# Optimization experiments

Measured on AMD Instinct MI355X. Metric: run time of the kernel, lower is better.

The kernel has to match this reference:

```python
import jax, jax.numpy as jnp
import numpy as np
from jax import lax

T, B, M, N, D, DA, H, W = 32, 8, 256, 256, 684, 512, 12, 48
QC_CH = 512  # hard-coded coverage conv channels in the module


def setup_inputs() -> dict:
    key = jax.random.key(0)
    ks = iter(jax.random.split(key, 64))
    f = lambda shape, s=0.05: jax.random.normal(next(ks), shape, dtype=jnp.float32) * s
    inp = {
        'rembedding': f((T, B, M), 1.0),
        're_embedding': f((T, B, M), 1.0),
        'ly_mask': jnp.ones((T, B), jnp.float32),
        'context': f((B, D, H, W), 1.0),
        'context_mask': jnp.ones((B, H, W), jnp.float32),
        'init_state': f((B, N), 1.0),
        # fc_Wyz/Wyr/Wyh : Linear(2m -> n)
        'Wyz_w': f((N, 2 * M)), 'Wyz_b': jnp.zeros((N,), jnp.float32),
        'Wyr_w': f((N, 2 * M)), 'Wyr_b': jnp.zeros((N,), jnp.float32),
        'Wyh_w': f((N, 2 * M)), 'Wyh_b': jnp.zeros((N,), jnp.float32),
        # fc_Uhz0/Uhr0/Uhh0 : Linear(n -> n, bias=False)
        'Uhz0_w': f((N, N)), 'Uhr0_w': f((N, N)), 'Uhh0_w': f((N, N)),
        # conv_UaC : Conv2d(D, da, 1)
        'UaC_w': f((DA, D)), 'UaC_b': jnp.zeros((DA,), jnp.float32),
        # fc_WaC : Linear(n -> da, bias=False)
        'WaC_w': f((DA, N)),
        # conv_QC : Conv2d(1, 512, 3, padding=1, bias=False)
        'QC_w': f((QC_CH, 1, 3, 3)),
        # fc_UfC : Linear(512 -> da)
        'UfC_w': f((DA, QC_CH)), 'UfC_b': jnp.zeros((DA,), jnp.float32),
        # fc_vaC : Linear(da -> 1)
        'vaC_w': f((1, DA)), 'vaC_b': jnp.zeros((1,), jnp.float32),
        # fc_Uhz2/Uhr2/Uhh2 : Linear(n -> n)
        'Uhz2_w': f((N, N)), 'Uhz2_b': jnp.zeros((N,), jnp.float32),
        'Uhr2_w': f((N, N)), 'Uhr2_b': jnp.zeros((N,), jnp.float32),
        'Uhh2_w': f((N, N)), 'Uhh2_b': jnp.zeros((N,), jnp.float32),
        # fc_Wcz/Wcr/Wch : Linear(D -> n, bias=False)
        'Wcz_w': f((N, D)), 'Wcr_w': f((N, D)), 'Wch_w': f((N, D)),
        # parent positions into the ctC buffer (valid parents are <= current step)
        'rp': jax.random.randint(next(ks), (T, B), 0, T, dtype=jnp.int32),
    }
    return inp


def _forward(rembedding, re_embedding, ly_mask, context, context_mask, init_state,
             Wyz_w, Wyz_b, Wyr_w, Wyr_b, Wyh_w, Wyh_b,
             Uhz0_w, Uhr0_w, Uhh0_w,
             UaC_w, UaC_b, WaC_w, QC_w, UfC_w, UfC_b, vaC_w, vaC_b,
             Uhz2_w, Uhz2_b, Uhr2_w, Uhr2_b, Uhh2_w, Uhh2_b,
             Wcz_w, Wcr_w, Wch_w, rp):
    n_steps, n_samples = rembedding.shape[0], rembedding.shape[1]
    Hc, Wc = context.shape[2], context.shape[3]
    n = init_state.shape[1]
    d = context.shape[1]

    # pctx_ = conv_UaC(context).permute(2,3,0,1)  -> [H, W, B, da]
    pctx = jnp.einsum('bdhw,ad->hwba', context, UaC_w) + UaC_b
    cmask = context_mask.transpose(1, 2, 0)  # [H, W, B]

    emb = jnp.concatenate([rembedding, re_embedding], axis=2)  # [T, B, 2m]
    sbz = emb @ Wyz_w.T + Wyz_b
    sbr = emb @ Wyr_w.T + Wyr_b
    sbh = emb @ Wyh_w.T + Wyh_b

    batch_idx = jnp.arange(n_samples)

    def step(carry, xs):
        h_, ap_, buf = carry  # h_: [B,n], ap_: [B,H,W], buf: [T+1,B,D]
        z_i, r_i, hh_i, lm, rpos, i = xs
        # gather parent contexts from the running ctC buffer (before this step)
        ctP = buf[rpos, batch_idx]  # [B, D]
        # first GRU cell
        z0 = jax.nn.sigmoid(h_ @ Uhz0_w.T + z_i)
        r0 = jax.nn.sigmoid(h_ @ Uhr0_w.T + r_i)
        h0p = jnp.tanh((h_ @ Uhh0_w.T) * r0 + hh_i)
        h0 = z0 * h_ + (1.0 - z0) * h0p
        h0 = lm[:, None] * h0 + (1.0 - lm)[:, None] * h_
        # coverage attention
        query = h0 @ WaC_w.T  # [B, da]
        cover = lax.conv_general_dilated(
            ap_[:, None, :, :], QC_w, (1, 1), ((1, 1), (1, 1)),
            dimension_numbers=('NCHW', 'OIHW', 'NCHW'))  # [B,512,H,W]
        ccov = jnp.einsum('bchw,ac->hwba', cover, UfC_w) + UfC_b  # [H,W,B,da]
        score = jnp.tanh(pctx + query[None, None, :, :] + ccov)  # [H,W,B,da]
        alpha = (score @ vaC_w.T + vaC_b)[..., 0]  # [H,W,B]
        alpha = jnp.exp(alpha - jnp.max(alpha))
        alpha = alpha * cmask
        alpha = alpha / jnp.sum(alpha, axis=(0, 1))[None, None, :] + 1e-10
        alpha_bhw = alpha.transpose(2, 0, 1)  # [B,H,W]
        ap = ap_ + alpha_bhw
        ctC = jnp.einsum('bdhw,bhw->bd', context, alpha_bhw)  # [B, D]
        # second GRU cell conditioned on the context vector
        z2 = jax.nn.sigmoid(h0 @ Uhz2_w.T + Uhz2_b + ctC @ Wcz_w.T)
        r2 = jax.nn.sigmoid(h0 @ Uhr2_w.T + Uhr2_b + ctC @ Wcr_w.T)
        h2p = jnp.tanh((h0 @ Uhh2_w.T + Uhh2_b) * r2 + ctC @ Wch_w.T)
        h2 = z2 * h0 + (1.0 - z2) * h2p
        h2 = lm[:, None] * h2 + (1.0 - lm)[:, None] * h0
        buf = lax.dynamic_update_slice_in_dim(buf, ctC[None], i + 1, axis=0)
        return (h2, ap, buf), (h2, ctC, ctP, alpha_bhw, ap)

    ap0 = jnp.zeros((n_samples, Hc, Wc), rembedding.dtype)
    buf0 = jnp.zeros((n_steps + 1, n_samples, d), rembedding.dtype)
    xs = (sbz, sbr, sbh, ly_mask, rp, jnp.arange(n_steps))
    _, (h2ts, ctCs, ctPs, calphas, calpha_pasts) = lax.scan(
        step, (init_state, ap0, buf0), xs)
    return h2ts, ctCs, ctPs, calphas, calpha_pasts


def reference(rembedding, re_embedding, ly_mask, context, context_mask, init_state,
              Wyz_w, Wyz_b, Wyr_w, Wyr_b, Wyh_w, Wyh_b,
              Uhz0_w, Uhr0_w, Uhh0_w,
              UaC_w, UaC_b, WaC_w, QC_w, UfC_w, UfC_b, vaC_w, vaC_b,
              Uhz2_w, Uhz2_b, Uhr2_w, Uhr2_b, Uhh2_w, Uhh2_b,
              Wcz_w, Wcr_w, Wch_w, rp):
    return _forward(rembedding, re_embedding, ly_mask, context, context_mask, init_state,
                    Wyz_w, Wyz_b, Wyr_w, Wyr_b, Wyh_w, Wyh_b,
                    Uhz0_w, Uhr0_w, Uhh0_w,
                    UaC_w, UaC_b, WaC_w, QC_w, UfC_w, UfC_b, vaC_w, vaC_b,
                    Uhz2_w, Uhz2_b, Uhr2_w, Uhr2_b, Uhh2_w, Uhh2_b,
                    Wcz_w, Wcr_w, Wch_w, rp)
```

## Files before the change

### kernel.cpp

```cpp
#include <hip/hip_runtime.h>
#include <stdint.h>

typedef unsigned short u16;
typedef unsigned int   u32;

#define TB_ 8
#define NN_ 256
#define DD_ 684
#define PP_ 576

#define OFF_SB    0u
#define OFF_TRAN  0u
#define OFF_BUF   786432u
#define OFF_PCTX  1486848u
#define OFF_FKT   10924032u
#define OFF_RAWP  10942464u
#define OFF_H     11237376u
#define OFF_H0    11245568u
#define OFF_EAL   11253760u
#define OFF_SYNC  11272192u
#define OFF_FLG   11276288u
#define WS_NEED   11276304u

#define OFF_H2   0
// ... 198 lines not shown
    const void* __restrict__ Wh, const void* __restrict__ bhh,
    float* __restrict__ sb,
    float* __restrict__ buf, u32* __restrict__ sync, float* __restrict__ h,
    const void* __restrict__ init_state,
    const int* __restrict__ flag)
{
  const int f32 = flag[0];
  const int tid = threadIdx.x;
  int bid = blockIdx.x;
  if (bid < 768){
    __shared__ float emb[512];
    int g = bid >> 8;
    int tb = bid & 255; int t = tb >> 3; int b = tb & 7;
    emb[tid]     = gld(remb,   (size_t)(t*8+b)*256 + tid, f32);
    emb[tid+256] = gld(re_emb, (size_t)(t*8+b)*256 + tid, f32);
    __syncthreads();
    const void* W = (g==0?Wz:(g==1?Wr:Wh));
    const void* bias = (g==0?bz:(g==1?br:bhh));
    float acc = gld(bias, tid, f32) + dotw(W, (size_t)tid*512, emb, 512, f32);
    sb[(((size_t)g*32+t)*8+b)*256 + tid] = acc;
    return;
  }
  bid -= 768;
  {
    int i = bid*256 + tid;
    int stride = 256*256;
    for (int k=i; k<32*TB_*DD_; k+=stride) buf[k] = 0.f;
    for (int k=i; k<TB_*128;    k+=stride) sync[k] = 0u;
    for (int k=i; k<TB_*NN_;    k+=stride) h[k]   = gld(init_state, k, f32);
  }
}


__global__ __launch_bounds__(256, 1) void k_main(
    const void* __restrict__ ly_mask, const void* __restrict__ context, const void* __restrict__ cmask,
    const void* __restrict__ Uhz0, const void* __restrict__ Uhr0, const void* __restrict__ Uhh0,
    const void* __restrict__ WaC, const void* __restrict__ vaC_w, const void* __restrict__ vaC_b,
    const void* __restrict__ Uhz2, const void* __restrict__ Uhz2_b,
    const void* __restrict__ Uhr2, const void* __restrict__ Uhr2_b,
    const void* __restrict__ Uhh2, const void* __restrict__ Uhh2_b,
    const void* __restrict__ Wcz, const void* __restrict__ Wcr, const void* __restrict__ Wch,
    const int* __restrict__ rp,
    const float* __restrict__ pctx, const float* __restrict__ sb, const float* __restrict__ FKt,
    float* buf, float* h_ws, float* h0_ws, float* rawp, u32* syncg,
    float* out, const int* __restrict__ flag)
{
  const int f32 = flag[0];
  const int tid = threadIdx.x;
  const int b = blockIdx.x >> 4;
  const int j = blockIdx.x & 15;
  const int abase = j*32, nbase = j*16;

  __shared__ float hprev[NN_], h0_lds[NN_];
  __shared__ float ap_lds[PP_], al_lds[PP_], cm_lds[PP_];
  __shared__ float ctc_lds[DD_];
  __shared__ float fk_lds[9*32], vac_lds[32], q_lds[32], qpart[256];
  __shared__ float g1[48], u2l[48], wcl[48];
  __shared__ float red[4];

  for (int k=tid; k<288; k+=256) fk_lds[k] = FKt[(k>>5)*512 + abase + (k&31)];
  if (tid < 32) vac_lds[tid] = gld(vaC_w, abase + tid, f32);
  cm_lds[tid]     = gld(cmask, b*PP_ + tid, f32);
  cm_lds[tid+256] = gld(cmask, b*PP_ + tid + 256, f32);
  if (tid < 64) cm_lds[tid+512] = gld(cmask, b*PP_ + tid + 512, f32);
  ap_lds[tid] = 0.f; ap_lds[tid+256] = 0.f;
  if (tid < 64) ap_lds[tid+512] = 0.f;
  const float vb = gld(vaC_b, 0, f32);

  u32* ctr = syncg + b*128;
  u32 bar_t = 0;
  const int p0 = tid, p1 = tid + 256, p2 = tid + 512;
  const bool has3 = (tid < 64);
  const int pown = j*36;

  for (int t=0; t<32; t++){
    const float lm = gld(ly_mask, t*8+b, f32);

    hprev[tid] = aload(&h_ws[b*256 + tid]);
    __syncthreads();
    if (tid < 192){
      int item = tid >> 2, q = tid & 3;
      int g = item >> 4, nl = item & 15;
      int n = nbase + nl;
      const void* U = (g==0 ? Uhz0 : (g==1 ? Uhr0 : Uhh0));
      float acc = dotw(U, (size_t)n*256 + q*64, &hprev[q*64], 64, f32);
      acc += __shfl_xor(acc,1,64); acc += __shfl_xor(acc,2,64);
      if (q==0) g1[g*16+nl] = acc;
    }
    __syncthreads();
    if (tid < 16){
      int n = nbase + tid;
      float hp = hprev[n];
      float z0 = sigm(g1[tid]    + sb[(((size_t)t)*8+b)*256 + n]);
      float r0 = sigm(g1[16+tid] + sb[(((size_t)(32+t))*8+b)*256 + n]);
      float hc = tanh_c(g1[32+tid]*r0 + sb[(((size_t)(64+t))*8+b)*256 + n]);
      float h0v = z0*hp + (1.f - z0)*hc;
      h0v = lm*h0v + (1.f - lm)*hp;
      astore(&h0_ws[b*256 + n], h0v);
    }
    {
      int rpos = rp[t*8+b];
      if ((unsigned)rpos > 31u) rpos = 31;
      int dbase = j*43, dcnt = (j==15) ? 39 : 43;
      if (tid < dcnt){
        int d = dbase + tid;
        out[OFF_CTP + (t*8+b)*DD_ + d] = aload(&buf[((size_t)rpos*8+b)*DD_ + d]);
      }
    }
    bar_t += 16; group_bar(ctr, bar_t);

    h0_lds[tid] = aload(&h0_ws[b*256 + tid]);
    __syncthreads();
    {
      int ai = tid & 31, nb = tid >> 5;
      qpart[nb*32 + ai] = dotw(WaC, (size_t)(abase+ai)*256 + nb*32, &h0_lds[nb*32], 32, f32);
    }
    __syncthreads();
    if (tid < 32){
      float qv = 0.f;
      #pragma unroll
      for (int nb2=0;nb2<8;nb2++) qv += qpart[nb2*32 + tid];
      q_lds[tid] = qv;
    }
    __syncthreads();
    for (int rep=0; rep<3; rep++){
      int p = tid + rep*256;
      if (p >= PP_) break;
      float PQ[32];
      const float* pc = pctx + ((size_t)(b*PP_ + p))*512 + abase;
      #pragma unroll
      for (int q8=0;q8<8;q8++){
        float4 u = *(const float4*)(pc + q8*4);
        PQ[q8*4+0]=u.x; PQ[q8*4+1]=u.y; PQ[q8*4+2]=u.z; PQ[q8*4+3]=u.w;
      }
      int hh_ = p / 48, ww_ = p - hh_*48;
      #pragma unroll
      for (int kh=0;kh<3;kh++){
        int h2_ = hh_ + kh - 1;
        if ((unsigned)h2_ >= 12u) continue;
        #pragma unroll
        for (int kw=0;kw<3;kw++){
          int w2_ = ww_ + kw - 1;
          if ((unsigned)w2_ >= 48u) continue;
          float av = ap_lds[h2_*48 + w2_];
          const float* fkp = &fk_lds[(kh*3+kw)*32];
          #pragma unroll
          for (int ai=0;ai<32;ai++) PQ[ai] = fmaf(av, fkp[ai], PQ[ai]);
        }
      }
      float racc = 0.f;
      #pragma unroll
      for (int ai=0;ai<32;ai++)
        racc = fmaf(vac_lds[ai], tanh_c(PQ[ai] + q_lds[ai]), racc);
      astore(&rawp[((size_t)(b*16+j))*PP_ + p], racc);
    }
    if (tid < 192){
      int item = tid >> 2, q = tid & 3;
      int g = item >> 4, nl = item & 15;
      int n = nbase + nl;
      const void* U = (g==0 ? Uhz2 : (g==1 ? Uhr2 : Uhh2));
      float acc = dotw(U, (size_t)n*256 + q*64, &h0_lds[q*64], 64, f32);
      acc += __shfl_xor(acc,1,64); acc += __shfl_xor(acc,2,64);
      if (q==0) u2l[g*16+nl] = acc;
    }
    bar_t += 16; group_bar(ctr, bar_t);

    {
      float psum = 0.f;
      for (int rep=0; rep<3; rep++){
        int p = tid + rep*256;
        if (p >= PP_) break;
        float raw = vb;
        #pragma unroll
        for (int j2=0;j2<16;j2++) raw += aload(&rawp[((size_t)(b*16+j2))*PP_ + p]);
        raw = fminf(fmaxf(raw, -60.f), 60.f);
        float e = __expf(raw) * cm_lds[p];
        al_lds[p] = e; psum += e;
      }
      #pragma unroll
      for (int off=1; off<64; off<<=1) psum += __shfl_xor(psum, off, 64);
      if ((tid & 63)==0) red[tid>>6] = psum;
    }
    __syncthreads();
    {
      float S = red[0] + red[1] + red[2] + red[3];
      S = fmaxf(S, 1e-30f);
      float inv = rcpf(S);
      float a0 = al_lds[p0]*inv + 1e-10f; al_lds[p0] = a0; ap_lds[p0] += a0;
      float a1 = al_lds[p1]*inv + 1e-10f; al_lds[p1] = a1; ap_lds[p1] += a1;
      if (has3){ float a2 = al_lds[p2]*inv + 1e-10f; al_lds[p2] = a2; ap_lds[p2] += a2; }
    }
    __syncthreads();
    if (tid < 36){
      int p = pown + tid;
      out[OFF_AL  + (t*8+b)*PP_ + p] = al_lds[p];
      out[OFF_APO + (t*8+b)*PP_ + p] = ap_lds[p];
    }
    {
      int dbase = j*43, dcnt = (j==15) ? 39 : 43;
      if (tid < dcnt*4){
        int dd = tid >> 2, q = tid & 3, d = dbase + dd;
        float acc;
        if (f32) acc = dotf((const float*)context + ((size_t)(b*DD_+d))*PP_ + q*144, &al_lds[q*144], 144);
        else {
          const u16* crow = (const u16*)context + ((size_t)(b*DD_+d))*PP_ + q*144;
          acc = 0.f;
          #pragma unroll 6
          for (int k=0;k<144;k+=8) acc += dot8(*(const uint4*)(crow+k), &al_lds[q*144+k]);
        }
        acc += __shfl_xor(acc,1,64); acc += __shfl_xor(acc,2,64);
        if (q==0){
          astore(&out[OFF_CTC + (t*8+b)*DD_ + d], acc);
          if (t < 31) astore(&buf[(((size_t)(t+1))*8+b)*DD_ + d], acc);
        }
      }
    }
    bar_t += 16; group_bar(ctr, bar_t);

    for (int k=tid; k<DD_; k+=256) ctc_lds[k] = aload(&out[OFF_CTC + (t*8+b)*DD_ + k]);
    __syncthreads();
    if (tid < 192){
      int item = tid >> 2, q = tid & 3;
      int g = item >> 4, nl = item & 15;
      int n = nbase + nl;
      const void* W = (g==0 ? Wcz : (g==1 ? Wcr : Wch));
      int base = q*176, cnt = (q==3) ? 156 : 176;
      float acc = dotw(W, (size_t)n*DD_ + base, &ctc_lds[base], cnt, f32);
      acc += __shfl_xor(acc,1,64); acc += __shfl_xor(acc,2,64);
      if (q==0) wcl[g*16+nl] = acc;
    }
    __syncthreads();
    if (tid < 16){
      int n = nbase + tid;
      float h0v = h0_lds[n];
      float z2 = sigm(u2l[tid]    + gld(Uhz2_b, n, f32) + wcl[tid]);
      float r2 = sigm(u2l[16+tid] + gld(Uhr2_b, n, f32) + wcl[16+tid]);
      float hc = tanh_c((u2l[32+tid] + gld(Uhh2_b, n, f32))*r2 + wcl[32+tid]);
      float h2v = z2*h0v + (1.f - z2)*hc;
      h2v = lm*h2v + (1.f - lm)*h0v;
      astore(&h_ws[b*256 + n], h2v);
      out[OFF_H2 + (t*8+b)*256 + n] = h2v;
    }
    bar_t += 16; group_bar(ctr, bar_t);
  }
}


extern "C" void kernel_launch(void* const* d_in, const int* in_sizes, int n_in,
                              void* d_out, int out_size, void* d_ws, size_t ws_size,
                              hipStream_t stream){
  (void)in_sizes; (void)n_in; (void)out_size;
  if (ws_size < WS_NEED) return;

  const void* remb       = d_in[0];
  const void* re_emb     = d_in[1];
  const void* ly_mask    = d_in[2];
  const void* context    = d_in[3];
  const void* cmask      = d_in[4];
  const void* init_state = d_in[5];
  const void* Wyz_w = d_in[6];  const void* Wyz_b = d_in[7];
  const void* Wyr_w = d_in[8];  const void* Wyr_b = d_in[9];
  const void* Wyh_w = d_in[10]; const void* Wyh_b = d_in[11];
  const void* Uhz0  = d_in[12];
  const void* Uhr0  = d_in[13];
  const void* Uhh0  = d_in[14];
  const void* UaC_w = d_in[15]; const void* UaC_b = d_in[16];
  const void* WaC_w = d_in[17];
  const void* QC_w  = d_in[18];
  const void* UfC_w = d_in[19]; const void* UfC_b = d_in[20];
  const void* vaC_w = d_in[21]; const void* vaC_b = d_in[22];
  const void* Uhz2  = d_in[23]; const void* Uhz2_b = d_in[24];
  const void* Uhr2  = d_in[25]; const void* Uhr2_b = d_in[26];
  const void* Uhh2  = d_in[27]; const void* Uhh2_b = d_in[28];
  const void* Wcz   = d_in[29];
  const void* Wcr   = d_in[30];
  const void* Wch   = d_in[31];
  const int*  rp    = (const int*)d_in[32];

  char* ws = (char*)d_ws;
  float* sbp   = (float*)(ws + OFF_SB);
  float* UaCT  = (float*)(ws + OFF_TRAN);
  float* buf   = (float*)(ws + OFF_BUF);
  float* pctx  = (float*)(ws + OFF_PCTX);
  float* FKt   = (float*)(ws + OFF_FKT);
  float* rawp  = (float*)(ws + OFF_RAWP);
  float* h_ws  = (float*)(ws + OFF_H);
  float* h0_ws = (float*)(ws + OFF_H0);
  u32*   syncg = (u32*)  (ws + OFF_SYNC);
  int*   flag  = (int*)  (ws + OFF_FLG);
  float* out   = (float*)d_out;

  k_detect<<<1, 256, 0, stream>>>((const u16*)context, flag);
  k_pre1 <<<120, 256, 0, stream>>>(UaC_w, UaCT, QC_w, UfC_w, FKt, flag);
  k_pctx2<<<144, 256, 0, stream>>>(context, UaCT, UaC_b, UfC_b, pctx, flag);
  k_pre2 <<<1024, 256, 0, stream>>>(remb, re_emb, Wyz_w, Wyz_b, Wyr_w, Wyr_b, Wyh_w, Wyh_b, sbp,
                                    buf, syncg, h_ws, init_state, flag);
  k_main <<<128, 256, 0, stream>>>(ly_mask, context, cmask,
                                   Uhz0, Uhr0, Uhh0, WaC_w, vaC_w, vaC_b,
                                   Uhz2, Uhz2_b, Uhr2, Uhr2_b, Uhh2, Uhh2_b,
                                   Wcz, Wcr, Wch, rp,
                                   pctx, sbp, FKt,
                                   buf, h_ws, h0_ws, rawp, syncg, out, flag);
}
```

Before: 1.190 ms.

## Use 4 blocks of 1024 threads per batch to cut cross-block barrier participants

The persistent recurrent kernel changes from 16 blocks of 256 threads per batch item to 4 blocks of 1024 threads. Each block now covers 128 attention dims, 64 hidden units and 171 context dims. The parent-context copy is folded into the first GEMV phase, and the softmax reduction uses 9 waves. The aim is to reduce the cost of the global group barriers (4 arrivals instead of 16) and to give each block more parallel work per step. In exchange, only 32 CUs are used and each block is much larger, which may raise per-CU latency and limit registers per thread.

```diff
diff --git a/kernel.cpp b/kernel.cpp
--- a/kernel.cpp
+++ b/kernel.cpp
@@ -254,7 +254,7 @@
 }
 
 
-__global__ __launch_bounds__(256, 1) void k_main(
+__global__ __launch_bounds__(1024, 1) void k_main(
     const void* __restrict__ ly_mask, const void* __restrict__ context, const void* __restrict__ cmask,
     const void* __restrict__ Uhz0, const void* __restrict__ Uhr0, const void* __restrict__ Uhh0,
     const void* __restrict__ WaC, const void* __restrict__ vaC_w, const void* __restrict__ vaC_b,
@@ -269,87 +269,83 @@
 {
   const int f32 = flag[0];
   const int tid = threadIdx.x;
-  const int b = blockIdx.x >> 4;
-  const int j = blockIdx.x & 15;
-  const int abase = j*32, nbase = j*16;
+  const int b = blockIdx.x >> 2;
+  const int j = blockIdx.x & 3;
+  const int abase = j*128;
+  const int nbase = j*64;
+  const int dbase = j*171;
 
   __shared__ float hprev[NN_], h0_lds[NN_];
   __shared__ float ap_lds[PP_], al_lds[PP_], cm_lds[PP_];
   __shared__ float ctc_lds[DD_];
-  __shared__ float fk_lds[9*32], vac_lds[32], q_lds[32], qpart[256];
-  __shared__ float g1[48], u2l[48], wcl[48];
-  __shared__ float red[4];
-
-  for (int k=tid; k<288; k+=256) fk_lds[k] = FKt[(k>>5)*512 + abase + (k&31)];
-  if (tid < 32) vac_lds[tid] = gld(vaC_w, abase + tid, f32);
-  cm_lds[tid]     = gld(cmask, b*PP_ + tid, f32);
-  cm_lds[tid+256] = gld(cmask, b*PP_ + tid + 256, f32);
-  if (tid < 64) cm_lds[tid+512] = gld(cmask, b*PP_ + tid + 512, f32);
-  ap_lds[tid] = 0.f; ap_lds[tid+256] = 0.f;
-  if (tid < 64) ap_lds[tid+512] = 0.f;
+  __shared__ float fk_lds[9*128], vac_lds[128], q_lds[128], qpart[1024];
+  __shared__ float g1[192], u2l[192], wcl[192];
+  __shared__ float red16[16];
+
+  for (int k=tid; k<9*128; k+=1024) fk_lds[k] = FKt[(k>>7)*512 + abase + (k&127)];
+  if (tid < 128) vac_lds[tid] = gld(vaC_w, abase + tid, f32);
+  if (tid < PP_){
+    cm_lds[tid] = gld(cmask, b*PP_ + tid, f32);
+    ap_lds[tid] = 0.f;
+  }
   const float vb = gld(vaC_b, 0, f32);
 
   u32* ctr = syncg + b*128;
   u32 bar_t = 0;
-  const int p0 = tid, p1 = tid + 256, p2 = tid + 512;
-  const bool has3 = (tid < 64);
-  const int pown = j*36;
 
   for (int t=0; t<32; t++){
     const float lm = gld(ly_mask, t*8+b, f32);
 
-    hprev[tid] = aload(&h_ws[b*256 + tid]);
-    __syncthreads();
-    if (tid < 192){
-      int item = tid >> 2, q = tid & 3;
-      int g = item >> 4, nl = item & 15;
+    if (tid < 256) hprev[tid] = aload(&h_ws[b*256 + tid]);
+    __syncthreads();
+    if (tid < 768){
+      int g = tid >> 8, rem = tid & 255;
+      int nl = rem >> 2, q = rem & 3;
       int n = nbase + nl;
       const void* U = (g==0 ? Uhz0 : (g==1 ? Uhr0 : Uhh0));
       float acc = dotw(U, (size_t)n*256 + q*64, &hprev[q*64], 64, f32);
       acc += __shfl_xor(acc,1,64); acc += __shfl_xor(acc,2,64);
-      if (q==0) g1[g*16+nl] = acc;
-    }
-    __syncthreads();
-    if (tid < 16){
+      if (q==0) g1[g*64+nl] = acc;
+    } else if (tid < 768+171){
+      int rpos = rp[t*8+b];
+      if ((unsigned)rpos > 31u) rpos = 31;
+      int d = dbase + (tid - 768);
+      out[OFF_CTP + (t*8+b)*DD_ + d] = aload(&buf[((size_t)rpos*8+b)*DD_ + d]);
+    }
+    __syncthreads();
+    if (tid < 64){
       int n = nbase + tid;
       float hp = hprev[n];
-      float z0 = sigm(g1[tid]    + sb[(((size_t)t)*8+b)*256 + n]);
-      float r0 = sigm(g1[16+tid] + sb[(((size_t)(32+t))*8+b)*256 + n]);
-      float hc = tanh_c(g1[32+tid]*r0 + sb[(((size_t)(64+t))*8+b)*256 + n]);
+      float z0 = sigm(g1[tid]     + sb[(((size_t)t)*8+b)*256 + n]);
+      float r0 = sigm(g1[64+tid]  + sb[(((size_t)(32+t))*8+b)*256 + n]);
+      float hc = tanh_c(g1[128+tid]*r0 + sb[(((size_t)(64+t))*8+b)*256 + n]);
       float h0v = z0*hp + (1.f - z0)*hc;
       h0v = lm*h0v + (1.f - lm)*hp;
       astore(&h0_ws[b*256 + n], h0v);
     }
+    bar_t += 4; group_bar(ctr, bar_t);
+
+    if (tid < 256) h0_lds[tid] = aload(&h0_ws[b*256 + tid]);
+    __syncthreads();
     {
-      int rpos = rp[t*8+b];
-      if ((unsigned)rpos > 31u) rpos = 31;
-      int dbase = j*43, dcnt = (j==15) ? 39 : 43;
-      if (tid < dcnt){
-        int d = dbase + tid;
-        out[OFF_CTP + (t*8+b)*DD_ + d] = aload(&buf[((size_t)rpos*8+b)*DD_ + d]);
-      }
-    }
-    bar_t += 16; group_bar(ctr, bar_t);
-
-    h0_lds[tid] = aload(&h0_ws[b*256 + tid]);
-    __syncthreads();
-    {
-      int ai = tid & 31, nb = tid >> 5;
-      qpart[nb*32 + ai] = dotw(WaC, (size_t)(abase+ai)*256 + nb*32, &h0_lds[nb*32], 32, f32);
-    }
-    __syncthreads();
-    if (tid < 32){
+      int nb = tid >> 7, ai = tid & 127;
+      qpart[nb*128 + ai] = dotw(WaC, (size_t)(abase+ai)*256 + nb*32, &h0_lds[nb*32], 32, f32);
+    }
+    __syncthreads();
+    if (tid < 128){
       float qv = 0.f;
       #pragma unroll
-      for (int nb2=0;nb2<8;nb2++) qv += qpart[nb2*32 + tid];
+      for (int nb2=0;nb2<8;nb2++) qv += qpart[nb2*128 + tid];
       q_lds[tid] = qv;
     }
     __syncthreads();
-    for (int rep=0; rep<3; rep++){
-      int p = tid + rep*256;
-      if (p >= PP_) break;
+    for (int round=0; round<3; round++){
+      int item = tid + round*1024;
+      if (item >= 2304) break;
+      int p = item >> 2, vs = item & 3;
+      int alb = vs*32;
       float PQ[32];
-      const float* pc = pctx + ((size_t)(b*PP_ + p))*512 + abase;
+      const float* pc = pctx + ((size_t)(b*PP_ + p))*512 + abase + alb;
       #pragma unroll
       for (int q8=0;q8<8;q8++){
         float4 u = *(const float4*)(pc + q8*4);
@@ -365,105 +361,106 @@
           int w2_ = ww_ + kw - 1;
           if ((unsigned)w2_ >= 48u) continue;
           float av = ap_lds[h2_*48 + w2_];
-          const float* fkp = &fk_lds[(kh*3+kw)*32];
+          const float* fkp = &fk_lds[(kh*3+kw)*128 + alb];
           #pragma unroll
           for (int ai=0;ai<32;ai++) PQ[ai] = fmaf(av, fkp[ai], PQ[ai]);
         }
       }
+      const float* ql = &q_lds[alb];
+      const float* vl = &vac_lds[alb];
       float racc = 0.f;
       #pragma unroll
       for (int ai=0;ai<32;ai++)
-        racc = fmaf(vac_lds[ai], tanh_c(PQ[ai] + q_lds[ai]), racc);
-      astore(&rawp[((size_t)(b*16+j))*PP_ + p], racc);
-    }
-    if (tid < 192){
-      int item = tid >> 2, q = tid & 3;
-      int g = item >> 4, nl = item & 15;
+        racc = fmaf(vl[ai], tanh_c(PQ[ai] + ql[ai]), racc);
+      astore(&rawp[((size_t)(b*16 + j*4 + vs))*PP_ + p], racc);
+    }
+    if (tid < 768){
+      int g = tid >> 8, rem = tid & 255;
+      int nl = rem >> 2, q = rem & 3;
       int n = nbase + nl;
       const void* U = (g==0 ? Uhz2 : (g==1 ? Uhr2 : Uhh2));
       float acc = dotw(U, (size_t)n*256 + q*64, &h0_lds[q*64], 64, f32);
       acc += __shfl_xor(acc,1,64); acc += __shfl_xor(acc,2,64);
-      if (q==0) u2l[g*16+nl] = acc;
-    }
-    bar_t += 16; group_bar(ctr, bar_t);
+      if (q==0) u2l[g*64+nl] = acc;
+    }
+    bar_t += 4; group_bar(ctr, bar_t);
 
     {
-      float psum = 0.f;
-      for (int rep=0; rep<3; rep++){
-        int p = tid + rep*256;
-        if (p >= PP_) break;
+      float ev = 0.f;
+      if (tid < PP_){
         float raw = vb;
         #pragma unroll
-        for (int j2=0;j2<16;j2++) raw += aload(&rawp[((size_t)(b*16+j2))*PP_ + p]);
+        for (int j2=0;j2<16;j2++) raw += aload(&rawp[((size_t)(b*16+j2))*PP_ + tid]);
         raw = fminf(fmaxf(raw, -60.f), 60.f);
-        float e = __expf(raw) * cm_lds[p];
-        al_lds[p] = e; psum += e;
-      }
-      #pragma unroll
-      for (int off=1; off<64; off<<=1) psum += __shfl_xor(psum, off, 64);
-      if ((tid & 63)==0) red[tid>>6] = psum;
-    }
-    __syncthreads();
-    {
-      float S = red[0] + red[1] + red[2] + red[3];
+        ev = __expf(raw) * cm_lds[tid];
+        al_lds[tid] = ev;
+      }
+      if (tid < 576){
+        float s = ev;
+        #pragma unroll
+        for (int off=1; off<64; off<<=1) s += __shfl_xor(s, off, 64);
+        if ((tid & 63)==0) red16[tid>>6] = s;
+      }
+    }
+    __syncthreads();
+    if (tid < PP_){
+      float S = 0.f;
+      #pragma unroll
+      for (int k=0;k<9;k++) S += red16[k];
       S = fmaxf(S, 1e-30f);
       float inv = rcpf(S);
-      float a0 = al_lds[p0]*inv + 1e-10f; al_lds[p0] = a0; ap_lds[p0] += a0;
-      float a1 = al_lds[p1]*inv + 1e-10f; al_lds[p1] = a1; ap_lds[p1] += a1;
-      if (has3){ float a2 = al_lds[p2]*inv + 1e-10f; al_lds[p2] = a2; ap_lds[p2] += a2; }
-    }
-    __syncthreads();
-    if (tid < 36){
-      int p = pown + tid;
+      float av = al_lds[tid]*inv + 1e-10f;
+      al_lds[tid] = av; ap_lds[tid] += av;
+    }
+    __syncthreads();
+    if (tid < 144){
+      int p = j*144 + tid;
       out[OFF_AL  + (t*8+b)*PP_ + p] = al_lds[p];
       out[OFF_APO + (t*8+b)*PP_ + p] = ap_lds[p];
     }
-    {
-      int dbase = j*43, dcnt = (j==15) ? 39 : 43;
-      if (tid < dcnt*4){
-        int dd = tid >> 2, q = tid & 3, d = dbase + dd;
-        float acc;
-        if (f32) acc = dotf((const float*)context + ((size_t)(b*DD_+d))*PP_ + q*144, &al_lds[q*144], 144);
-        else {
-          const u16* crow = (const u16*)context + ((size_t)(b*DD_+d))*PP_ + q*144;
-          acc = 0.f;
-          #pragma unroll 6
-          for (int k=0;k<144;k+=8) acc += dot8(*(const uint4*)(crow+k), &al_lds[q*144+k]);
-        }
-        acc += __shfl_xor(acc,1,64); acc += __shfl_xor(acc,2,64);
-        if (q==0){
-          astore(&out[OFF_CTC + (t*8+b)*DD_ + d], acc);
-          if (t < 31) astore(&buf[(((size_t)(t+1))*8+b)*DD_ + d], acc);
-        }
-      }
-    }
-    bar_t += 16; group_bar(ctr, bar_t);
-
-    for (int k=tid; k<DD_; k+=256) ctc_lds[k] = aload(&out[OFF_CTC + (t*8+b)*DD_ + k]);
-    __syncthreads();
-    if (tid < 192){
-      int item = tid >> 2, q = tid & 3;
-      int g = item >> 4, nl = item & 15;
+    if (tid < 684){
+      int dd = tid >> 2, q = tid & 3, d = dbase + dd;
+      float acc;
+      if (f32) acc = dotf((const float*)context + ((size_t)(b*DD_+d))*PP_ + q*144, &al_lds[q*144], 144);
+      else {
+        const u16* crow = (const u16*)context + ((size_t)(b*DD_+d))*PP_ + q*144;
+        acc = 0.f;
+        #pragma unroll 6
+        for (int k=0;k<144;k+=8) acc += dot8(*(const uint4*)(crow+k), &al_lds[q*144+k]);
+      }
+      acc += __shfl_xor(acc,1,64); acc += __shfl_xor(acc,2,64);
+      if (q==0){
+        astore(&out[OFF_CTC + (t*8+b)*DD_ + d], acc);
+        if (t < 31) astore(&buf[(((size_t)(t+1))*8+b)*DD_ + d], acc);
+      }
+    }
+    bar_t += 4; group_bar(ctr, bar_t);
+
+    if (tid < DD_) ctc_lds[tid] = aload(&out[OFF_CTC + (t*8+b)*DD_ + tid]);
+    __syncthreads();
+    if (tid < 768){
+      int g = tid >> 8, rem = tid & 255;
+      int nl = rem >> 2, q = rem & 3;
       int n = nbase + nl;
       const void* W = (g==0 ? Wcz : (g==1 ? Wcr : Wch));
-      int base = q*176, cnt = (q==3) ? 156 : 176;
+      int base = q*172, cnt = (q==3) ? 168 : 172;
       float acc = dotw(W, (size_t)n*DD_ + base, &ctc_lds[base], cnt, f32);
       acc += __shfl_xor(acc,1,64); acc += __shfl_xor(acc,2,64);
-      if (q==0) wcl[g*16+nl] = acc;
-    }
-    __syncthreads();
-    if (tid < 16){
+      if (q==0) wcl[g*64+nl] = acc;
+    }
+    __syncthreads();
+    if (tid < 64){
       int n = nbase + tid;
       float h0v = h0_lds[n];
-      float z2 = sigm(u2l[tid]    + gld(Uhz2_b, n, f32) + wcl[tid]);
-      float r2 = sigm(u2l[16+tid] + gld(Uhr2_b, n, f32) + wcl[16+tid]);
-      float hc = tanh_c((u2l[32+tid] + gld(Uhh2_b, n, f32))*r2 + wcl[32+tid]);
+      float z2 = sigm(u2l[tid]     + gld(Uhz2_b, n, f32) + wcl[tid]);
+      float r2 = sigm(u2l[64+tid]  + gld(Uhr2_b, n, f32) + wcl[64+tid]);
+      float hc = tanh_c((u2l[128+tid] + gld(Uhh2_b, n, f32))*r2 + wcl[128+tid]);
       float h2v = z2*h0v + (1.f - z2)*hc;
       h2v = lm*h2v + (1.f - lm)*h0v;
       astore(&h_ws[b*256 + n], h2v);
       out[OFF_H2 + (t*8+b)*256 + n] = h2v;
     }
-    bar_t += 16; group_bar(ctr, bar_t);
+    bar_t += 4; group_bar(ctr, bar_t);
   }
 }
 
@@ -517,7 +514,7 @@
   k_pctx2<<<144, 256, 0, stream>>>(context, UaCT, UaC_b, UfC_b, pctx, flag);
   k_pre2 <<<1024, 256, 0, stream>>>(remb, re_emb, Wyz_w, Wyz_b, Wyr_w, Wyr_b, Wyh_w, Wyh_b, sbp,
                                     buf, syncg, h_ws, init_state, flag);
-  k_main <<<128, 256, 0, stream>>>(ly_mask, context, cmask,
+  k_main <<<32, 1024, 0, stream>>>(ly_mask, context, cmask,
                                    Uhz0, Uhr0, Uhh0, WaC_w, vaC_w, vaC_b,
                                    Uhz2, Uhz2_b, Uhr2, Uhr2_b, Uhh2, Uhh2_b,
                                    Wcz, Wcr, Wch, rp,
```

Result: slower. 2.813 ms (+136.3%).

## Shrink per-batch block group from 16 to 4 and drop two grid barriers

Applied to the files above, without the earlier changes.

Each batch element now runs on 4 cooperating blocks instead of 16, so the main kernel launches 32 blocks. Every block redundantly computes the full first GRU stage and the full context vector, which removes two of the four cross-block group barriers per timestep. The aim is to cut inter-block sync latency in this latency-bound recurrent loop. The cost is more serial work per block: full 256-length dot products per thread, 9 attention rounds instead of 3, and full 576-length context reductions, all on far fewer CUs.

```diff
diff --git a/kernel.cpp b/kernel.cpp
--- a/kernel.cpp
+++ b/kernel.cpp
@@ -264,24 +264,26 @@
     const void* __restrict__ Wcz, const void* __restrict__ Wcr, const void* __restrict__ Wch,
     const int* __restrict__ rp,
     const float* __restrict__ pctx, const float* __restrict__ sb, const float* __restrict__ FKt,
-    float* buf, float* h_ws, float* h0_ws, float* rawp, u32* syncg,
+    float* buf, float* h_ws, float* rawp, u32* syncg,
     float* out, const int* __restrict__ flag)
 {
   const int f32 = flag[0];
   const int tid = threadIdx.x;
-  const int b = blockIdx.x >> 4;
-  const int j = blockIdx.x & 15;
-  const int abase = j*32, nbase = j*16;
+  const int b = blockIdx.x >> 2;
+  const int j = blockIdx.x & 3;
+  const int abase = j*128;
+  const int nbase = j*64;
+  const int dbase = j*171;
 
   __shared__ float hprev[NN_], h0_lds[NN_];
   __shared__ float ap_lds[PP_], al_lds[PP_], cm_lds[PP_];
   __shared__ float ctc_lds[DD_];
-  __shared__ float fk_lds[9*32], vac_lds[32], q_lds[32], qpart[256];
-  __shared__ float g1[48], u2l[48], wcl[48];
+  __shared__ float fk_lds[9*128], vac_lds[128], q_lds[128], qpart[256];
+  __shared__ float u2l[192], wcl[192];
   __shared__ float red[4];
 
-  for (int k=tid; k<288; k+=256) fk_lds[k] = FKt[(k>>5)*512 + abase + (k&31)];
-  if (tid < 32) vac_lds[tid] = gld(vaC_w, abase + tid, f32);
+  for (int k=tid; k<9*128; k+=256) fk_lds[k] = FKt[(k>>7)*512 + abase + (k&127)];
+  if (tid < 128) vac_lds[tid] = gld(vaC_w, abase + tid, f32);
   cm_lds[tid]     = gld(cmask, b*PP_ + tid, f32);
   cm_lds[tid+256] = gld(cmask, b*PP_ + tid + 256, f32);
   if (tid < 64) cm_lds[tid+512] = gld(cmask, b*PP_ + tid + 512, f32);
@@ -293,63 +295,45 @@
   u32 bar_t = 0;
   const int p0 = tid, p1 = tid + 256, p2 = tid + 512;
   const bool has3 = (tid < 64);
-  const int pown = j*36;
 
   for (int t=0; t<32; t++){
     const float lm = gld(ly_mask, t*8+b, f32);
 
     hprev[tid] = aload(&h_ws[b*256 + tid]);
     __syncthreads();
-    if (tid < 192){
-      int item = tid >> 2, q = tid & 3;
-      int g = item >> 4, nl = item & 15;
-      int n = nbase + nl;
-      const void* U = (g==0 ? Uhz0 : (g==1 ? Uhr0 : Uhh0));
-      float acc = dotw(U, (size_t)n*256 + q*64, &hprev[q*64], 64, f32);
-      acc += __shfl_xor(acc,1,64); acc += __shfl_xor(acc,2,64);
-      if (q==0) g1[g*16+nl] = acc;
-    }
-    __syncthreads();
-    if (tid < 16){
-      int n = nbase + tid;
-      float hp = hprev[n];
-      float z0 = sigm(g1[tid]    + sb[(((size_t)t)*8+b)*256 + n]);
-      float r0 = sigm(g1[16+tid] + sb[(((size_t)(32+t))*8+b)*256 + n]);
-      float hc = tanh_c(g1[32+tid]*r0 + sb[(((size_t)(64+t))*8+b)*256 + n]);
+    {
+      float az = dotw(Uhz0, (size_t)tid*256, hprev, 256, f32);
+      float ar = dotw(Uhr0, (size_t)tid*256, hprev, 256, f32);
+      float ah = dotw(Uhh0, (size_t)tid*256, hprev, 256, f32);
+      float hp = hprev[tid];
+      float z0 = sigm(az + sb[(((size_t)t)*8+b)*256 + tid]);
+      float r0 = sigm(ar + sb[(((size_t)(32+t))*8+b)*256 + tid]);
+      float hc = tanh_c(ah*r0 + sb[(((size_t)(64+t))*8+b)*256 + tid]);
       float h0v = z0*hp + (1.f - z0)*hc;
-      h0v = lm*h0v + (1.f - lm)*hp;
-      astore(&h0_ws[b*256 + n], h0v);
-    }
-    {
+      h0_lds[tid] = lm*h0v + (1.f - lm)*hp;
+    }
+    if (tid < 171){
       int rpos = rp[t*8+b];
       if ((unsigned)rpos > 31u) rpos = 31;
-      int dbase = j*43, dcnt = (j==15) ? 39 : 43;
-      if (tid < dcnt){
-        int d = dbase + tid;
-        out[OFF_CTP + (t*8+b)*DD_ + d] = aload(&buf[((size_t)rpos*8+b)*DD_ + d]);
-      }
-    }
-    bar_t += 16; group_bar(ctr, bar_t);
-
-    h0_lds[tid] = aload(&h0_ws[b*256 + tid]);
-    __syncthreads();
+      int d = dbase + tid;
+      out[OFF_CTP + (t*8+b)*DD_ + d] = aload(&buf[((size_t)rpos*8+b)*DD_ + d]);
+    }
+    __syncthreads();
+
     {
-      int ai = tid & 31, nb = tid >> 5;
-      qpart[nb*32 + ai] = dotw(WaC, (size_t)(abase+ai)*256 + nb*32, &h0_lds[nb*32], 32, f32);
-    }
-    __syncthreads();
-    if (tid < 32){
-      float qv = 0.f;
-      #pragma unroll
-      for (int nb2=0;nb2<8;nb2++) qv += qpart[nb2*32 + tid];
-      q_lds[tid] = qv;
-    }
-    __syncthreads();
-    for (int rep=0; rep<3; rep++){
-      int p = tid + rep*256;
-      if (p >= PP_) break;
+      int ai = tid & 127, half = tid >> 7;
+      qpart[half*128 + ai] = dotw(WaC, (size_t)(abase+ai)*256 + half*128, &h0_lds[half*128], 128, f32);
+    }
+    __syncthreads();
+    if (tid < 128) q_lds[tid] = qpart[tid] + qpart[128+tid];
+    __syncthreads();
+    #pragma unroll 1
+    for (int round=0; round<9; round++){
+      int item = tid + round*256;
+      int p = item >> 2, vs = item & 3;
+      int alb = vs*32;
       float PQ[32];
-      const float* pc = pctx + ((size_t)(b*PP_ + p))*512 + abase;
+      const float* pc = pctx + ((size_t)(b*PP_ + p))*512 + abase + alb;
       #pragma unroll
       for (int q8=0;q8<8;q8++){
         float4 u = *(const float4*)(pc + q8*4);
@@ -365,27 +349,26 @@
           int w2_ = ww_ + kw - 1;
           if ((unsigned)w2_ >= 48u) continue;
           float av = ap_lds[h2_*48 + w2_];
-          const float* fkp = &fk_lds[(kh*3+kw)*32];
+          const float* fkp = &fk_lds[(kh*3+kw)*128 + alb];
           #pragma unroll
           for (int ai=0;ai<32;ai++) PQ[ai] = fmaf(av, fkp[ai], PQ[ai]);
         }
       }
+      const float* ql = &q_lds[alb];
+      const float* vl = &vac_lds[alb];
       float racc = 0.f;
       #pragma unroll
       for (int ai=0;ai<32;ai++)
-        racc = fmaf(vac_lds[ai], tanh_c(PQ[ai] + q_lds[ai]), racc);
-      astore(&rawp[((size_t)(b*16+j))*PP_ + p], racc);
+        racc = fmaf(vl[ai], tanh_c(PQ[ai] + ql[ai]), racc);
+      astore(&rawp[((size_t)(b*16 + j*4 + vs))*PP_ + p], racc);
     }
     if (tid < 192){
-      int item = tid >> 2, q = tid & 3;
-      int g = item >> 4, nl = item & 15;
+      int g = tid >> 6, nl = tid & 63;
       int n = nbase + nl;
       const void* U = (g==0 ? Uhz2 : (g==1 ? Uhr2 : Uhh2));
-      float acc = dotw(U, (size_t)n*256 + q*64, &h0_lds[q*64], 64, f32);
-      acc += __shfl_xor(acc,1,64); acc += __shfl_xor(acc,2,64);
-      if (q==0) u2l[g*16+nl] = acc;
-    }
-    bar_t += 16; group_bar(ctr, bar_t);
+      u2l[g*64+nl] = dotw(U, (size_t)n*256, h0_lds, 256, f32);
+    }
+    bar_t += 4; group_bar(ctr, bar_t);
 
     {
       float psum = 0.f;
@@ -413,57 +396,46 @@
       if (has3){ float a2 = al_lds[p2]*inv + 1e-10f; al_lds[p2] = a2; ap_lds[p2] += a2; }
     }
     __syncthreads();
-    if (tid < 36){
-      int p = pown + tid;
+    if (tid < 144){
+      int p = j*144 + tid;
       out[OFF_AL  + (t*8+b)*PP_ + p] = al_lds[p];
       out[OFF_APO + (t*8+b)*PP_ + p] = ap_lds[p];
     }
-    {
-      int dbase = j*43, dcnt = (j==15) ? 39 : 43;
-      if (tid < dcnt*4){
-        int dd = tid >> 2, q = tid & 3, d = dbase + dd;
-        float acc;
-        if (f32) acc = dotf((const float*)context + ((size_t)(b*DD_+d))*PP_ + q*144, &al_lds[q*144], 144);
-        else {
-          const u16* crow = (const u16*)context + ((size_t)(b*DD_+d))*PP_ + q*144;
-          acc = 0.f;
-          #pragma unroll 6
-          for (int k=0;k<144;k+=8) acc += dot8(*(const uint4*)(crow+k), &al_lds[q*144+k]);
-        }
-        acc += __shfl_xor(acc,1,64); acc += __shfl_xor(acc,2,64);
-        if (q==0){
-          astore(&out[OFF_CTC + (t*8+b)*DD_ + d], acc);
-          if (t < 31) astore(&buf[(((size_t)(t+1))*8+b)*DD_ + d], acc);
-        }
-      }
-    }
-    bar_t += 16; group_bar(ctr, bar_t);
-
-    for (int k=tid; k<DD_; k+=256) ctc_lds[k] = aload(&out[OFF_CTC + (t*8+b)*DD_ + k]);
+    for (int d = tid; d < DD_; d += 256){
+      float acc;
+      if (f32) acc = dotf((const float*)context + ((size_t)(b*DD_+d))*PP_, al_lds, PP_);
+      else {
+        const u16* crow = (const u16*)context + ((size_t)(b*DD_+d))*PP_;
+        acc = 0.f;
+        #pragma unroll 8
+        for (int k=0;k<PP_;k+=8) acc += dot8(*(const uint4*)(crow+k), &al_lds[k]);
+      }
+      ctc_lds[d] = acc;
+      if ((unsigned)(d - dbase) < 171u){
+        astore(&out[OFF_CTC + (t*8+b)*DD_ + d], acc);
+        if (t < 31) astore(&buf[(((size_t)(t+1))*8+b)*DD_ + d], acc);
+      }
+    }
     __syncthreads();
     if (tid < 192){
-      int item = tid >> 2, q = tid & 3;
-      int g = item >> 4, nl = item & 15;
+      int g = tid >> 6, nl = tid & 63;
       int n = nbase + nl;
       const void* W = (g==0 ? Wcz : (g==1 ? Wcr : Wch));
-      int base = q*176, cnt = (q==3) ? 156 : 176;
-      float acc = dotw(W, (size_t)n*DD_ + base, &ctc_lds[base], cnt, f32);
-      acc += __shfl_xor(acc,1,64); acc += __shfl_xor(acc,2,64);
-      if (q==0) wcl[g*16+nl] = acc;
-    }
-    __syncthreads();
-    if (tid < 16){
+      wcl[g*64+nl] = dotw(W, (size_t)n*DD_, ctc_lds, DD_, f32);
+    }
+    __syncthreads();
+    if (tid < 64){
       int n = nbase + tid;
       float h0v = h0_lds[n];
-      float z2 = sigm(u2l[tid]    + gld(Uhz2_b, n, f32) + wcl[tid]);
-      float r2 = sigm(u2l[16+tid] + gld(Uhr2_b, n, f32) + wcl[16+tid]);
-      float hc = tanh_c((u2l[32+tid] + gld(Uhh2_b, n, f32))*r2 + wcl[32+tid]);
+      float z2 = sigm(u2l[tid]     + gld(Uhz2_b, n, f32) + wcl[tid]);
+      float r2 = sigm(u2l[64+tid]  + gld(Uhr2_b, n, f32) + wcl[64+tid]);
+      float hc = tanh_c((u2l[128+tid] + gld(Uhh2_b, n, f32))*r2 + wcl[128+tid]);
       float h2v = z2*h0v + (1.f - z2)*hc;
       h2v = lm*h2v + (1.f - lm)*h0v;
       astore(&h_ws[b*256 + n], h2v);
       out[OFF_H2 + (t*8+b)*256 + n] = h2v;
     }
-    bar_t += 16; group_bar(ctr, bar_t);
+    bar_t += 4; group_bar(ctr, bar_t);
   }
 }
 
@@ -507,7 +479,6 @@
   float* FKt   = (float*)(ws + OFF_FKT);
   float* rawp  = (float*)(ws + OFF_RAWP);
   float* h_ws  = (float*)(ws + OFF_H);
-  float* h0_ws = (float*)(ws + OFF_H0);
   u32*   syncg = (u32*)  (ws + OFF_SYNC);
   int*   flag  = (int*)  (ws + OFF_FLG);
   float* out   = (float*)d_out;
@@ -517,10 +488,10 @@
   k_pctx2<<<144, 256, 0, stream>>>(context, UaCT, UaC_b, UfC_b, pctx, flag);
   k_pre2 <<<1024, 256, 0, stream>>>(remb, re_emb, Wyz_w, Wyz_b, Wyr_w, Wyr_b, Wyh_w, Wyh_b, sbp,
                                     buf, syncg, h_ws, init_state, flag);
-  k_main <<<128, 256, 0, stream>>>(ly_mask, context, cmask,
-                                   Uhz0, Uhr0, Uhh0, WaC_w, vaC_w, vaC_b,
-                                   Uhz2, Uhz2_b, Uhr2, Uhr2_b, Uhh2, Uhh2_b,
-                                   Wcz, Wcr, Wch, rp,
-                                   pctx, sbp, FKt,
-                                   buf, h_ws, h0_ws, rawp, syncg, out, flag);
-}
+  k_main <<<32, 256, 0, stream>>>(ly_mask, context, cmask,
+                                  Uhz0, Uhr0, Uhh0, WaC_w, vaC_w, vaC_b,
+                                  Uhz2, Uhz2_b, Uhr2, Uhr2_b, Uhh2, Uhh2_b,
+                                  Wcz, Wcr, Wch, rp,
+                                  pctx, sbp, FKt,
+                                  buf, h_ws, rawp, syncg, out, flag);
+}
```

After: 4.511 ms. 279% more time.

## Halve blocks per batch group and distribute softmax normalization via workspace

Applied to the files above, without the earlier changes.

Reduces the persistent recurrent kernel from 16 to 8 cooperating blocks per batch element, so each block handles twice as many hidden units, attention channels and context dims. Cross-block group barriers then involve fewer participants. The softmax exponentials are now computed once per position by the owning block and shared through a global buffer with partial sums, instead of every block recomputing all 576 positions. This adds a fourth group barrier per step and gives each block more serial work.

```diff
diff --git a/kernel.cpp b/kernel.cpp
--- a/kernel.cpp
+++ b/kernel.cpp
@@ -264,24 +264,27 @@
     const void* __restrict__ Wcz, const void* __restrict__ Wcr, const void* __restrict__ Wch,
     const int* __restrict__ rp,
     const float* __restrict__ pctx, const float* __restrict__ sb, const float* __restrict__ FKt,
-    float* buf, float* h_ws, float* h0_ws, float* rawp, u32* syncg,
+    float* buf, float* h_ws, float* h0_ws, float* ealpha, float* rawp, u32* syncg,
     float* out, const int* __restrict__ flag)
 {
   const int f32 = flag[0];
   const int tid = threadIdx.x;
-  const int b = blockIdx.x >> 4;
-  const int j = blockIdx.x & 15;
-  const int abase = j*32, nbase = j*16;
+  const int b = blockIdx.x >> 3;
+  const int j = blockIdx.x & 7;
+  const int abase = j*64, nbase = j*32;
+  const int dbase = j*85 + (j < 4 ? j : 4);
+  const int dcnt  = (j < 4) ? 86 : 85;
+  const int pown  = j*72;
 
   __shared__ float hprev[NN_], h0_lds[NN_];
   __shared__ float ap_lds[PP_], al_lds[PP_], cm_lds[PP_];
   __shared__ float ctc_lds[DD_];
-  __shared__ float fk_lds[9*32], vac_lds[32], q_lds[32], qpart[256];
-  __shared__ float g1[48], u2l[48], wcl[48];
-  __shared__ float red[4];
-
-  for (int k=tid; k<288; k+=256) fk_lds[k] = FKt[(k>>5)*512 + abase + (k&31)];
-  if (tid < 32) vac_lds[tid] = gld(vaC_w, abase + tid, f32);
+  __shared__ float fk_lds[9*64], vac_lds[64], q_lds[64], qpart[256];
+  __shared__ float g1[96], u2l[96], wcl[96];
+  __shared__ float red16[16];
+
+  for (int k=tid; k<9*64; k+=256) fk_lds[k] = FKt[(k>>6)*512 + abase + (k&63)];
+  if (tid < 64) vac_lds[tid] = gld(vaC_w, abase + tid, f32);
   cm_lds[tid]     = gld(cmask, b*PP_ + tid, f32);
   cm_lds[tid+256] = gld(cmask, b*PP_ + tid + 256, f32);
   if (tid < 64) cm_lds[tid+512] = gld(cmask, b*PP_ + tid + 512, f32);
@@ -290,10 +293,10 @@
   const float vb = gld(vaC_b, 0, f32);
 
   u32* ctr = syncg + b*128;
+  float* psum_ws = (float*)(ctr + 96);
   u32 bar_t = 0;
   const int p0 = tid, p1 = tid + 256, p2 = tid + 512;
   const bool has3 = (tid < 64);
-  const int pown = j*36;
 
   for (int t=0; t<32; t++){
     const float lm = gld(ly_mask, t*8+b, f32);
@@ -301,21 +304,21 @@
     hprev[tid] = aload(&h_ws[b*256 + tid]);
     __syncthreads();
     if (tid < 192){
-      int item = tid >> 2, q = tid & 3;
-      int g = item >> 4, nl = item & 15;
+      int item = tid >> 1, q = tid & 1;
+      int g = item >> 5, nl = item & 31;
       int n = nbase + nl;
       const void* U = (g==0 ? Uhz0 : (g==1 ? Uhr0 : Uhh0));
-      float acc = dotw(U, (size_t)n*256 + q*64, &hprev[q*64], 64, f32);
-      acc += __shfl_xor(acc,1,64); acc += __shfl_xor(acc,2,64);
-      if (q==0) g1[g*16+nl] = acc;
-    }
-    __syncthreads();
-    if (tid < 16){
+      float acc = dotw(U, (size_t)n*256 + q*128, &hprev[q*128], 128, f32);
+      acc += __shfl_xor(acc,1,64);
+      if (q==0) g1[g*32+nl] = acc;
+    }
+    __syncthreads();
+    if (tid < 32){
       int n = nbase + tid;
       float hp = hprev[n];
       float z0 = sigm(g1[tid]    + sb[(((size_t)t)*8+b)*256 + n]);
-      float r0 = sigm(g1[16+tid] + sb[(((size_t)(32+t))*8+b)*256 + n]);
-      float hc = tanh_c(g1[32+tid]*r0 + sb[(((size_t)(64+t))*8+b)*256 + n]);
+      float r0 = sigm(g1[32+tid] + sb[(((size_t)(32+t))*8+b)*256 + n]);
+      float hc = tanh_c(g1[64+tid]*r0 + sb[(((size_t)(64+t))*8+b)*256 + n]);
       float h0v = z0*hp + (1.f - z0)*hc;
       h0v = lm*h0v + (1.f - lm)*hp;
       astore(&h0_ws[b*256 + n], h0v);
@@ -323,33 +326,33 @@
     {
       int rpos = rp[t*8+b];
       if ((unsigned)rpos > 31u) rpos = 31;
-      int dbase = j*43, dcnt = (j==15) ? 39 : 43;
       if (tid < dcnt){
         int d = dbase + tid;
         out[OFF_CTP + (t*8+b)*DD_ + d] = aload(&buf[((size_t)rpos*8+b)*DD_ + d]);
       }
     }
-    bar_t += 16; group_bar(ctr, bar_t);
+    bar_t += 8; group_bar(ctr, bar_t);
 
     h0_lds[tid] = aload(&h0_ws[b*256 + tid]);
     __syncthreads();
     {
-      int ai = tid & 31, nb = tid >> 5;
-      qpart[nb*32 + ai] = dotw(WaC, (size_t)(abase+ai)*256 + nb*32, &h0_lds[nb*32], 32, f32);
-    }
-    __syncthreads();
-    if (tid < 32){
-      float qv = 0.f;
-      #pragma unroll
-      for (int nb2=0;nb2<8;nb2++) qv += qpart[nb2*32 + tid];
+      int ai = tid & 63, nb = tid >> 6;
+      qpart[nb*64 + ai] = dotw(WaC, (size_t)(abase+ai)*256 + nb*64, &h0_lds[nb*64], 64, f32);
+    }
+    __syncthreads();
+    if (tid < 64){
+      float qv = qpart[tid] + qpart[64+tid] + qpart[128+tid] + qpart[192+tid];
       q_lds[tid] = qv;
     }
     __syncthreads();
-    for (int rep=0; rep<3; rep++){
-      int p = tid + rep*256;
-      if (p >= PP_) break;
+    #pragma unroll 1
+    for (int round=0; round<5; round++){
+      int item = tid + round*256;
+      if (item >= 1152) break;
+      int p = item >> 1, vs = item & 1;
+      int alb = vs*32;
       float PQ[32];
-      const float* pc = pctx + ((size_t)(b*PP_ + p))*512 + abase;
+      const float* pc = pctx + ((size_t)(b*PP_ + p))*512 + abase + alb;
       #pragma unroll
       for (int q8=0;q8<8;q8++){
         float4 u = *(const float4*)(pc + q8*4);
@@ -365,105 +368,117 @@
           int w2_ = ww_ + kw - 1;
           if ((unsigned)w2_ >= 48u) continue;
           float av = ap_lds[h2_*48 + w2_];
-          const float* fkp = &fk_lds[(kh*3+kw)*32];
+          const float* fkp = &fk_lds[(kh*3+kw)*64 + alb];
           #pragma unroll
           for (int ai=0;ai<32;ai++) PQ[ai] = fmaf(av, fkp[ai], PQ[ai]);
         }
       }
+      const float* ql = &q_lds[alb];
+      const float* vl = &vac_lds[alb];
       float racc = 0.f;
       #pragma unroll
       for (int ai=0;ai<32;ai++)
-        racc = fmaf(vac_lds[ai], tanh_c(PQ[ai] + q_lds[ai]), racc);
-      astore(&rawp[((size_t)(b*16+j))*PP_ + p], racc);
+        racc = fmaf(vl[ai], tanh_c(PQ[ai] + ql[ai]), racc);
+      astore(&rawp[((size_t)(b*16 + j*2 + vs))*PP_ + p], racc);
     }
     if (tid < 192){
-      int item = tid >> 2, q = tid & 3;
-      int g = item >> 4, nl = item & 15;
+      int item = tid >> 1, q = tid & 1;
+      int g = item >> 5, nl = item & 31;
       int n = nbase + nl;
       const void* U = (g==0 ? Uhz2 : (g==1 ? Uhr2 : Uhh2));
-      float acc = dotw(U, (size_t)n*256 + q*64, &h0_lds[q*64], 64, f32);
-      acc += __shfl_xor(acc,1,64); acc += __shfl_xor(acc,2,64);
-      if (q==0) u2l[g*16+nl] = acc;
-    }
-    bar_t += 16; group_bar(ctr, bar_t);
+      float acc = dotw(U, (size_t)n*256 + q*128, &h0_lds[q*128], 128, f32);
+      acc += __shfl_xor(acc,1,64);
+      if (q==0) u2l[g*32+nl] = acc;
+    }
+    bar_t += 8; group_bar(ctr, bar_t);
 
     {
-      float psum = 0.f;
-      for (int rep=0; rep<3; rep++){
-        int p = tid + rep*256;
-        if (p >= PP_) break;
+      float ev = 0.f;
+      if (tid < 72){
+        int p = pown + tid;
         float raw = vb;
         #pragma unroll
         for (int j2=0;j2<16;j2++) raw += aload(&rawp[((size_t)(b*16+j2))*PP_ + p]);
         raw = fminf(fmaxf(raw, -60.f), 60.f);
-        float e = __expf(raw) * cm_lds[p];
-        al_lds[p] = e; psum += e;
-      }
-      #pragma unroll
-      for (int off=1; off<64; off<<=1) psum += __shfl_xor(psum, off, 64);
-      if ((tid & 63)==0) red[tid>>6] = psum;
-    }
-    __syncthreads();
+        ev = __expf(raw) * cm_lds[p];
+        astore(&ealpha[b*PP_ + p], ev);
+      }
+      if (tid < 128){
+        float s = ev;
+        #pragma unroll
+        for (int off=1; off<64; off<<=1) s += __shfl_xor(s, off, 64);
+        if ((tid & 63) == 0) astore(&psum_ws[j*2 + (tid>>6)], s);
+      }
+    }
+    bar_t += 8; group_bar(ctr, bar_t);
+
     {
-      float S = red[0] + red[1] + red[2] + red[3];
+      float e0 = aload(&ealpha[b*PP_ + p0]);
+      float e1 = aload(&ealpha[b*PP_ + p1]);
+      float e2 = has3 ? aload(&ealpha[b*PP_ + p2]) : 0.f;
+      if (tid < 16) red16[tid] = aload(&psum_ws[tid]);
+      __syncthreads();
+      float S = 0.f;
+      #pragma unroll
+      for (int k=0;k<16;k++) S += red16[k];
       S = fmaxf(S, 1e-30f);
       float inv = rcpf(S);
-      float a0 = al_lds[p0]*inv + 1e-10f; al_lds[p0] = a0; ap_lds[p0] += a0;
-      float a1 = al_lds[p1]*inv + 1e-10f; al_lds[p1] = a1; ap_lds[p1] += a1;
-      if (has3){ float a2 = al_lds[p2]*inv + 1e-10f; al_lds[p2] = a2; ap_lds[p2] += a2; }
-    }
-    __syncthreads();
-    if (tid < 36){
+      float a0 = e0*inv + 1e-10f; al_lds[p0] = a0; ap_lds[p0] += a0;
+      float a1 = e1*inv + 1e-10f; al_lds[p1] = a1; ap_lds[p1] += a1;
+      if (has3){ float a2 = e2*inv + 1e-10f; al_lds[p2] = a2; ap_lds[p2] += a2; }
+    }
+    __syncthreads();
+    if (tid < 72){
       int p = pown + tid;
       out[OFF_AL  + (t*8+b)*PP_ + p] = al_lds[p];
       out[OFF_APO + (t*8+b)*PP_ + p] = ap_lds[p];
     }
     {
-      int dbase = j*43, dcnt = (j==15) ? 39 : 43;
-      if (tid < dcnt*4){
-        int dd = tid >> 2, q = tid & 3, d = dbase + dd;
+      int dd = tid >> 1, q = tid & 1;
+      if (dd < dcnt){
+        int d = dbase + dd;
         float acc;
-        if (f32) acc = dotf((const float*)context + ((size_t)(b*DD_+d))*PP_ + q*144, &al_lds[q*144], 144);
+        if (f32) acc = dotf((const float*)context + ((size_t)(b*DD_+d))*PP_ + q*288, &al_lds[q*288], 288);
         else {
-          const u16* crow = (const u16*)context + ((size_t)(b*DD_+d))*PP_ + q*144;
+          const u16* crow = (const u16*)context + ((size_t)(b*DD_+d))*PP_ + q*288;
           acc = 0.f;
           #pragma unroll 6
-          for (int k=0;k<144;k+=8) acc += dot8(*(const uint4*)(crow+k), &al_lds[q*144+k]);
+          for (int k=0;k<288;k+=8) acc += dot8(*(const uint4*)(crow+k), &al_lds[q*288+k]);
         }
-        acc += __shfl_xor(acc,1,64); acc += __shfl_xor(acc,2,64);
+        acc += __shfl_xor(acc,1,64);
         if (q==0){
           astore(&out[OFF_CTC + (t*8+b)*DD_ + d], acc);
           if (t < 31) astore(&buf[(((size_t)(t+1))*8+b)*DD_ + d], acc);
         }
       }
     }
-    bar_t += 16; group_bar(ctr, bar_t);
+    bar_t += 8; group_bar(ctr, bar_t);
 
     for (int k=tid; k<DD_; k+=256) ctc_lds[k] = aload(&out[OFF_CTC + (t*8+b)*DD_ + k]);
     __syncthreads();
     if (tid < 192){
-      int item = tid >> 2, q = tid & 3;
-      int g = item >> 4, nl = item & 15;
+      int item = tid >> 1, q = tid & 1;
+      int g = item >> 5, nl = item & 31;
       int n = nbase + nl;
       const void* W = (g==0 ? Wcz : (g==1 ? Wcr : Wch));
-      int base = q*176, cnt = (q==3) ? 156 : 176;
+      int base = q*344, cnt = q ? 340 : 344;
       float acc = dotw(W, (size_t)n*DD_ + base, &ctc_lds[base], cnt, f32);
-      acc += __shfl_xor(acc,1,64); acc += __shfl_xor(acc,2,64);
-      if (q==0) wcl[g*16+nl] = acc;
-    }
-    __syncthreads();
-    if (tid < 16){
+      acc += __shfl_xor(acc,1,64);
+      if (q==0) wcl[g*32+nl] = acc;
+    }
+    __syncthreads();
+    if (tid < 32){
       int n = nbase + tid;
       float h0v = h0_lds[n];
       float z2 = sigm(u2l[tid]    + gld(Uhz2_b, n, f32) + wcl[tid]);
-      float r2 = sigm(u2l[16+tid] + gld(Uhr2_b, n, f32) + wcl[16+tid]);
-      float hc = tanh_c((u2l[32+tid] + gld(Uhh2_b, n, f32))*r2 + wcl[32+tid]);
+      float r2 = sigm(u2l[32+tid] + gld(Uhr2_b, n, f32) + wcl[32+tid]);
+      float hc = tanh_c((u2l[64+tid] + gld(Uhh2_b, n, f32))*r2 + wcl[64+tid]);
       float h2v = z2*h0v + (1.f - z2)*hc;
       h2v = lm*h2v + (1.f - lm)*h0v;
       astore(&h_ws[b*256 + n], h2v);
       out[OFF_H2 + (t*8+b)*256 + n] = h2v;
     }
-    bar_t += 16; group_bar(ctr, bar_t);
+    bar_t += 8; group_bar(ctr, bar_t);
   }
 }
 
@@ -508,6 +523,7 @@
   float* rawp  = (float*)(ws + OFF_RAWP);
   float* h_ws  = (float*)(ws + OFF_H);
   float* h0_ws = (float*)(ws + OFF_H0);
+  float* eal   = (float*)(ws + OFF_EAL);
   u32*   syncg = (u32*)  (ws + OFF_SYNC);
   int*   flag  = (int*)  (ws + OFF_FLG);
   float* out   = (float*)d_out;
@@ -517,10 +533,10 @@
   k_pctx2<<<144, 256, 0, stream>>>(context, UaCT, UaC_b, UfC_b, pctx, flag);
   k_pre2 <<<1024, 256, 0, stream>>>(remb, re_emb, Wyz_w, Wyz_b, Wyr_w, Wyr_b, Wyh_w, Wyh_b, sbp,
                                     buf, syncg, h_ws, init_state, flag);
-  k_main <<<128, 256, 0, stream>>>(ly_mask, context, cmask,
-                                   Uhz0, Uhr0, Uhh0, WaC_w, vaC_w, vaC_b,
-                                   Uhz2, Uhz2_b, Uhr2, Uhr2_b, Uhh2, Uhh2_b,
-                                   Wcz, Wcr, Wch, rp,
-                                   pctx, sbp, FKt,
-                                   buf, h_ws, h0_ws, rawp, syncg, out, flag);
-}
+  k_main <<<64, 256, 0, stream>>>(ly_mask, context, cmask,
+                                  Uhz0, Uhr0, Uhh0, WaC_w, vaC_w, vaC_b,
+                                  Uhz2, Uhz2_b, Uhr2, Uhr2_b, Uhh2, Uhh2_b,
+                                  Wcz, Wcr, Wch, rp,
+                                  pctx, sbp, FKt,
+                                  buf, h_ws, h0_ws, eal, rawp, syncg, out, flag);
+}
```

Result: slower. 1.588 ms (+33.4%).
